# Performance work log

Measured on AMD Instinct MI355X. Metric: run time of the kernel, lower is better.

The kernel has to match this reference:

```python
import jax, jax.numpy as jnp
import numpy as np

B, L, W = 64, 20, 48
D = W * W           # 2304, MoE input/output size (image_width**2)
E = 4               # num_experts
HID = 2 * D         # expert hidden size
K = 1               # top_k
LOSS_COEF = 1e-2


def _cv_squared(x):
    # torch: x.var() (unbiased) / (x.mean()**2 + eps)
    eps = 1e-10
    return jnp.var(x, ddof=1) / (jnp.mean(x) ** 2 + eps)


def _moe(x, w_gate, w1, b1, w2, b2):
    # Noisy top-k gating, inference path (train=False => clean logits, no noise).
    logits = x @ w_gate                                   # [B, E]
    top_logits, top_idx = jax.lax.top_k(logits, K + 1)    # min(k+1, E)
    topk_gates = jax.nn.softmax(top_logits[:, :K], axis=-1)
    gates = jnp.zeros_like(logits).at[
        jnp.arange(x.shape[0])[:, None], top_idx[:, :K]
    ].set(topk_gates)                                     # [B, E] sparse gates
    importance = gates.sum(0)
    load = (gates > 0).sum(0).astype(x.dtype)             # _gates_to_load
    aux = LOSS_COEF * (_cv_squared(importance) + _cv_squared(load))
    # Dense expert compute weighted by gates (same math as dispatch/combine).
    h = jax.nn.relu(jnp.einsum('bd,edh->beh', x, w1) + b1)      # [B,E,HID]
    y = jnp.einsum('beh,ehd->bed', h, w2) + b2                  # [B,E,D]
    out = jnp.einsum('be,bed->bd', gates, y)                    # [B,D]
    return out, aux


def _conv3d(x, w, b, pad):
    y = jax.lax.conv_general_dilated(
        x, w, window_strides=(1, 1, 1), padding=pad,
        dimension_numbers=('NCDHW', 'OIDHW', 'NCDHW'))
    return y + b[None, :, None, None, None]


def _forward(input, conv1_w, conv1_b, conv2_w, conv2_b,
             t_gate, t_w1, t_b1, t_w2, t_b2,
             a_gate, a_w1, a_b1, a_w2, a_b2,
             q_gate, q_w1, q_b1, q_w2, q_b2,
             enc_w, enc_b, dec_w, dec_b):
    x = jnp.transpose(input, (0, 2, 1, 3, 4))                   # [B,1,L,H,W]
    x = jax.nn.relu(_conv3d(x, conv1_w, conv1_b, ((1, 1), (1, 1), (1, 1))))
    x = jax.nn.relu(_conv3d(x, conv2_w, conv2_b, ((0, 0), (1, 1), (1, 1))))  # [B,1,1,H,W]
    xf = x.reshape(x.shape[0], -1)                              # [B, D]
    transform, l1 = _moe(xf, t_gate, t_w1, t_b1, t_w2, t_b2)
    add, l2 = _moe(xf, a_gate, a_w1, a_b1, a_w2, a_b2)
    quad, l3 = _moe(xf, q_gate, q_w1, q_b1, q_w2, q_b2)
    s = input.shape                                             # [B,L,1,H,W]
    transform = transform.reshape(s[0], 1, s[2], s[3], s[4])
    add = add.reshape(s[0], 1, s[2], s[3], s[4])
    quad = quad.reshape(s[0], 1, s[2], s[3], s[4])
    out = input * input * quad + input * transform + add        # [B,L,1,H,W]
    # encoder = Linear(D,D)+ReLU, decoder = Linear(D,D) over flattened H*W
    of = out.reshape(s[0], s[1], D)
    of = jax.nn.relu(of @ enc_w + enc_b)
    of = of @ dec_w + dec_b
    of = jax.nn.sigmoid(of)
    return of.reshape(s), l1 + l2 + l3


def setup_inputs() -> dict:
    key = jax.random.key(0)
    ks = jax.random.split(key, 32)
    sc = 0.02
    inp = {
        'input': jax.random.normal(ks[0], (B, L, 1, W, W), jnp.float32),
        'conv1_w': jax.random.normal(ks[1], (10, 1, 3, 3, 3), jnp.float32) * sc,
        'conv1_b': jnp.zeros((10,), jnp.float32),
        'conv2_w': jax.random.normal(ks[2], (1, 10, L, 3, 3), jnp.float32) * sc,
        'conv2_b': jnp.zeros((1,), jnp.float32),
        'enc_w': jax.random.normal(ks[3], (D, D), jnp.float32) * sc,
        'enc_b': jnp.zeros((D,), jnp.float32),
        'dec_w': jax.random.normal(ks[4], (D, D), jnp.float32) * sc,
        'dec_b': jnp.zeros((D,), jnp.float32),
    }
    for i, p in enumerate(['t', 'a', 'q']):
        k0, k1, k2 = jax.random.split(ks[5 + i], 3)
        inp[p + '_gate'] = jnp.zeros((D, E), jnp.float32) + jax.random.normal(k0, (D, E), jnp.float32) * sc
        inp[p + '_w1'] = jax.random.normal(k1, (E, D, HID), jnp.float32) * sc
        inp[p + '_b1'] = jnp.zeros((E, HID), jnp.float32)
        inp[p + '_w2'] = jax.random.normal(k2, (E, HID, D), jnp.float32) * sc
        inp[p + '_b2'] = jnp.zeros((E, D), jnp.float32)
    return inp


def reference(input, conv1_w, conv1_b, conv2_w, conv2_b,
              t_gate, t_w1, t_b1, t_w2, t_b2,
              a_gate, a_w1, a_b1, a_w2, a_b2,
              q_gate, q_w1, q_b1, q_w2, q_b2,
              enc_w, enc_b, dec_w, dec_b):
    return _forward(input, conv1_w, conv1_b, conv2_w, conv2_b,
                    t_gate, t_w1, t_b1, t_w2, t_b2,
                    a_gate, a_w1, a_b1, a_w2, a_b2,
                    q_gate, q_w1, q_b1, q_w2, q_b2,
                    enc_w, enc_b, dec_w, dec_b)
```

## Files before the change

kernel.cpp:

```cpp
#include <hip/hip_runtime.h>
#include <stdint.h>

#define NB 64
#define NL 20
#define ND 2304
#define NE 4
#define NH 4608
#define NM 1280

typedef float f32x4 __attribute__((ext_vector_type(4)));
typedef __bf16 bf16x8 __attribute__((ext_vector_type(8)));
typedef unsigned short u16;
typedef u16 u16x4 __attribute__((ext_vector_type(4)));
typedef unsigned int u32;
typedef u32 u32x4 __attribute__((ext_vector_type(4)));

__device__ __forceinline__ u16 f2bf(float f) {
  u32 u = __builtin_bit_cast(u32, f);
  u += 0x7fffu + ((u >> 16) & 1u);
  return (u16)(u >> 16);
}

__device__ __forceinline__ void gl_lds16(const void* g, void* l) {
  __builtin_amdgcn_global_load_lds(
      (const __attribute__((address_space(1))) void*)g,
      (__attribute__((address_space(3))) void*)l, 16, 0, 0);
}

#define OFF_XFACC 0
#define OFF_XF    147456
#define OFF_H     294912
#define OFF_Y     1179648
#define OFF_AUX   1622016
#define OFF_CNT   1622020
#define OFF_ROWS  1622032
#define OFF_OFB   1622240
#define OFF_H1B   3096800
#define OFF_ENCWB 4571360
#define OFF_DECWB 7225568
#define OFF_XC    9879776
#define OFF_P     10322144

__global__ __launch_bounds__(256) void k_zero(float* __restrict__ p) {
  p[(size_t)blockIdx.x * 256 + threadIdx.x] = 0.f;
}

__global__ __launch_bounds__(256) void k_conv(
    const float* __restrict__ in, const float* __restrict__ w1,
    const float* __restrict__ b1, const float* __restrict__ w2,
    float* __restrict__ xf_acc) {
  __shared__ float insl[3][50][50];
  __shared__ float c1[2][50][50];
  __shared__ float w1s[270];
  __shared__ float w2s[90];
  __shared__ float b1s[10];
  const int d = blockIdx.x, b = blockIdx.y, t = threadIdx.x;
  for (int i = t; i < 270; i += 256) w1s[i] = w1[i];
  for (int i = t; i < 90; i += 256) w2s[i] = w2[(size_t)((i / 9) * 20 + d) * 9 + (i % 9)];
  if (t < 10) b1s[t] = b1[t];
  for (int i = t; i < 7500; i += 256) {
    int s = i / 2500, rr = (i % 2500) / 50, cc = i % 50;
    int gd = d - 1 + s, gy = rr - 1, gx = cc - 1;
    float v = 0.f;
    if (gd >= 0 && gd < NL && (unsigned)gy < 48u && (unsigned)gx < 48u)
      v = in[((size_t)b * NL + gd) * ND + gy * 48 + gx];
    insl[s][rr][cc] = v;
  }
  for (int i = t; i < 5000; i += 256) ((float*)c1)[i] = 0.f;
  float s2[3][4];
#pragma unroll
  for (int qi = 0; qi < 3; ++qi)
#pragma unroll
    for (int xq = 0; xq < 4; ++xq) s2[qi][xq] = 0.f;
  __syncthreads();
  for (int pc = 0; pc < 5; ++pc) {
#pragma unroll
    for (int qi = 0; qi < 3; ++qi) {
      int q = t + qi * 256;
      if (q < 576) {
        int y = q / 12, x0 = (q % 12) * 4;
        float a0[4], a1[4];
        const float bb0 = b1s[2 * pc], bb1 = b1s[2 * pc + 1];
#pragma unroll
        for (int xq = 0; xq < 4; ++xq) { a0[xq] = bb0; a1[xq] = bb1; }
#pragma unroll
        for (int kd = 0; kd < 3; ++kd)
#pragma unroll
          for (int ky = 0; ky < 3; ++ky) {
            float v[6];
#pragma unroll
            for (int i = 0; i < 6; ++i) v[i] = insl[kd][y + ky][x0 + i];
            const float* wa = &w1s[(2 * pc) * 27 + kd * 9 + ky * 3];
            const float* wb = wa + 27;
#pragma unroll
            for (int xq = 0; xq < 4; ++xq) {
              a0[xq] += v[xq] * wa[0] + v[xq + 1] * wa[1] + v[xq + 2] * wa[2];
              a1[xq] += v[xq] * wb[0] + v[xq + 1] * wb[1] + v[xq + 2] * wb[2];
            }
          }
#pragma unroll
        for (int xq = 0; xq < 4; ++xq) {
          c1[0][y + 1][x0 + 1 + xq] = fmaxf(a0[xq], 0.f);
          c1[1][y + 1][x0 + 1 + xq] = fmaxf(a1[xq], 0.f);
        }
      }
    }
    __syncthreads();
#pragma unroll
    for (int qi = 0; qi < 3; ++qi) {
      int q = t + qi * 256;
      if (q < 576) {
        int y = q / 12, x0 = (q % 12) * 4;
#pragma unroll
        for (int cc = 0; cc < 2; ++cc) {
#pragma unroll
          for (int ky = 0; ky < 3; ++ky) {
            float v[6];
#pragma unroll
            for (int i = 0; i < 6; ++i) v[i] = c1[cc][y + ky][x0 + i];
            const float* wr = &w2s[(2 * pc + cc) * 9 + ky * 3];
#pragma unroll
            for (int xq = 0; xq < 4; ++xq)
              s2[qi][xq] += v[xq] * wr[0] + v[xq + 1] * wr[1] + v[xq + 2] * wr[2];
          }
        }
      }
    }
    __syncthreads();
  }
#pragma unroll
  for (int qi = 0; qi < 3; ++qi) {
    int q = t + qi * 256;
    if (q < 576) {
#pragma unroll
      for (int xq = 0; xq < 4; ++xq)
        atomicAdd(&xf_acc[(size_t)b * ND + q * 4 + xq], s2[qi][xq]);
    }
  }
}

__global__ __launch_bounds__(256) void k_bias_relu(
    const float* __restrict__ acc, const float* __restrict__ c2b, float* __restrict__ xf) {
  size_t i = (size_t)blockIdx.x * 256 + threadIdx.x;
  xf[i] = fmaxf(acc[i] + c2b[0], 0.f);
}

__global__ __launch_bounds__(256) void k_gate(
    const float* __restrict__ xf,
    const float* __restrict__ g0, const float* __restrict__ g1, const float* __restrict__ g2,
    float* __restrict__ aux, int* __restrict__ cnt, int* __restrict__ rows) {
  const int p = blockIdx.x, t = threadIdx.x;
  const float* __restrict__ g = (p == 0) ? g0 : ((p == 1) ? g1 : g2);
  __shared__ float lg[64][4];
  __shared__ int lidx[64];
  __shared__ int lcnt[4];
  if (t < 4) lcnt[t] = 0;
  const int wv = t >> 6, l = t & 63;
  for (int b0 = 0; b0 < 64; b0 += 4) {
    int bb = b0 + wv;
    f32x4 acc = {0.f, 0.f, 0.f, 0.f};
    const float* xr = xf + (size_t)bb * ND + l * 36;
    const float* gr = g + (size_t)l * 36 * 4;
#pragma unroll
    for (int i4 = 0; i4 < 9; ++i4) {
      f32x4 xv = *(const f32x4*)(xr + i4 * 4);
#pragma unroll
      for (int qq = 0; qq < 4; ++qq) {
        f32x4 gv = *(const f32x4*)(gr + (i4 * 4 + qq) * 4);
        acc += xv[qq] * gv;
      }
    }
#pragma unroll
    for (int e = 0; e < 4; ++e) {
      float pv = acc[e];
#pragma unroll
      for (int off = 32; off > 0; off >>= 1) pv += __shfl_down(pv, off);
      if (l == 0) lg[bb][e] = pv;
    }
  }
  __syncthreads();
  if (t < 64) {
    float best = lg[t][0];
    int bi = 0;
#pragma unroll
    for (int e = 1; e < 4; ++e)
      if (lg[t][e] > best) { best = lg[t][e]; bi = e; }
    lidx[t] = bi;
    atomicAdd(&lcnt[bi], 1);
  }
  __syncthreads();
  if (t == 0) {
    int ofs[4]; int run = 0;
#pragma unroll
    for (int e = 0; e < 4; ++e) { ofs[e] = run; run += lcnt[e]; cnt[p * 4 + e] = lcnt[e]; }
    for (int b = 0; b < 64; ++b) { int e = lidx[b]; rows[p * 64 + ofs[e]++] = b; }
    float var = 0.f;
#pragma unroll
    for (int e = 0; e < 4; ++e) { float dd = (float)lcnt[e] - 16.f; var += dd * dd; }
    var *= (1.f / 3.f);
    aux[p] = 0.02f * var / (256.f + 1e-10f);
  }
}

__global__ __launch_bounds__(256) void k_gather(
    const float* __restrict__ xf, const int* __restrict__ rows, u16* __restrict__ Xb) {
  const int slot = blockIdx.x, t = threadIdx.x;
  const int r = rows[slot];
  const f32x4* src = (const f32x4*)(xf + (size_t)r * ND);
  u16x4* dst = (u16x4*)(Xb + (size_t)slot * ND);
  for (int i = t; i < ND / 4; i += 256) {
    f32x4 v = src[i];
    u16x4 o;
#pragma unroll
    for (int q = 0; q < 4; ++q) o[q] = f2bf(v[q]);
    dst[i] = o;
  }
}

template <int K, int N, int KS>
__global__ __launch_bounds__(256) void k_moe_mfma(
    const u16* __restrict__ Xb,
    const float* __restrict__ wt, const float* __restrict__ wa, const float* __restrict__ wq,
    const int* __restrict__ cnt, float* __restrict__ P) {
  constexpr int KL = K / KS;
  constexpr int NT = KL / 32;
  const int tile = blockIdx.x;
  const int ks = blockIdx.y;
  const int pe = blockIdx.z >> 1, ch = blockIdx.z & 1;
  const int p = pe >> 2, e = pe & 3;
  const int c = cnt[p * 4 + e];
  const int rstart = ch * 32;
  if (rstart >= c) return;
  const int nrows = min(32, c - rstart);
  int pref = 0;
  for (int e2 = 0; e2 < e; ++e2) pref += cnt[p * 4 + e2];
  const int slot0 = p * 64 + pref + rstart;
  const float* __restrict__ W = (p == 0) ? wt : ((p == 1) ? wa : wq);
  __shared__ u16 xs[32 * 296];
  __shared__ u16 Bs[2][128 * 40];
  const int t = threadIdx.x;
  const int w = t >> 6, l = t & 63;
  const int l15 = l & 15, l4 = l >> 4;

  if (l < 36) {
#pragma unroll
    for (int rr = 0; rr < 8; ++rr) {
      const int r = w * 8 + rr;
      int slot = slot0 + r; if (slot > 191) slot = 191;
      gl_lds16(Xb + (size_t)slot * K + ks * KL + l * 8, &xs[r * 296]);
    }
  }

  const int wk = t >> 3;
  const int wn = (t & 7) * 16;
  const float* Wg = W + (size_t)e * K * N + ((size_t)(ks * KL + wk)) * N + tile * 128 + wn;

  f32x4 rbuf[2][4];
#define LOADW(BUF, KT)                                                        \
  { _Pragma("unroll")                                                         \
    for (int q = 0; q < 4; ++q)                                               \
      rbuf[BUF][q] = *(const f32x4*)(Wg + (size_t)(KT) * 32 * N + q * 4); }
#define CVTW(BUF, DBUF)                                                       \
  { _Pragma("unroll")                                                         \
    for (int q = 0; q < 4; ++q) {                                             \
      _Pragma("unroll")                                                       \
      for (int j = 0; j < 4; ++j) {                                           \
        const int n_ = wn + q * 4 + j;                                        \
        const int pk_ = wk ^ (((n_ >> 4) & 3) << 3);                          \
        Bs[DBUF][n_ * 40 + pk_] = f2bf(rbuf[BUF][q][j]);                      \
      } } }

  f32x4 acc[4] = {};
  const int mbase = (w & 1) * 16;
  const int nql = (w >> 1) * 64;

  LOADW(0, 0);
  CVTW(0, 0);
  LOADW(1, 1);
  __syncthreads();

#pragma unroll
  for (int kt = 0; kt < NT; ++kt) {
    const bf16x8 af = *(const bf16x8*)&xs[(mbase + l15) * 296 + kt * 32 + l4 * 8];
#pragma unroll
    for (int i = 0; i < 4; ++i) {
      const int s = ((((w >> 1) * 4 + i)) & 3) << 3;
      const bf16x8 bf = *(const bf16x8*)&Bs[kt & 1][(nql + i * 16 + l15) * 40 + ((l4 * 8) ^ s)];
      acc[i] = __builtin_amdgcn_mfma_f32_16x16x32_bf16(af, bf, acc[i], 0, 0, 0);
    }
    if (kt + 1 < NT) { CVTW((kt + 1) & 1, (kt + 1) & 1); }
    if (kt + 2 < NT) { LOADW(kt & 1, kt + 2); }
    __syncthreads();
  }
#undef LOADW
#undef CVTW

  const size_t pbase = (size_t)ks * 192 * N;
#pragma unroll
  for (int i = 0; i < 4; ++i) {
    const int n = tile * 128 + nql + i * 16 + l15;
#pragma unroll
    for (int r = 0; r < 4; ++r) {
      const int m = mbase + l4 * 4 + r;
      if (m < nrows) P[pbase + (size_t)(slot0 + m) * N + n] = acc[i][r];
    }
  }
}

__global__ __launch_bounds__(256) void k_red1(
    const float* __restrict__ P,
    const float* __restrict__ b1t, const float* __restrict__ b1a, const float* __restrict__ b1q,
    const int* __restrict__ cnt, u16* __restrict__ Hb) {
  const int slot = blockIdx.y;
  const int p = slot >> 6, pos = slot & 63;
  int e = 0, run = cnt[p * 4];
  while (pos >= run && e < 3) { ++e; run += cnt[p * 4 + e]; }
  const float* __restrict__ b1 = (p == 0) ? b1t : ((p == 1) ? b1a : b1q);
  const int j0 = blockIdx.x * 1024 + threadIdx.x * 4;
  if (j0 >= NH) return;
  f32x4 s = *(const f32x4*)(b1 + (size_t)e * NH + j0);
#pragma unroll
  for (int ks = 0; ks < 8; ++ks)
    s += *(const f32x4*)(P + ((size_t)ks * 192 + slot) * NH + j0);
  u16x4 o;
#pragma unroll
  for (int q = 0; q < 4; ++q) o[q] = f2bf(fmaxf(s[q], 0.f));
  *(u16x4*)(Hb + (size_t)slot * NH + j0) = o;
}

__global__ __launch_bounds__(256) void k_red2(
    const float* __restrict__ P,
    const float* __restrict__ b2t, const float* __restrict__ b2a, const float* __restrict__ b2q,
    const int* __restrict__ cnt, const int* __restrict__ rows, float* __restrict__ Y) {
  const int slot = blockIdx.y;
  const int p = slot >> 6, pos = slot & 63;
  int e = 0, run = cnt[p * 4];
  while (pos >= run && e < 3) { ++e; run += cnt[p * 4 + e]; }
  const float* __restrict__ b2 = (p == 0) ? b2t : ((p == 1) ? b2a : b2q);
  const int b = rows[slot];
  const int t = threadIdx.x;
  if (t >= 192) return;
  const int j0 = blockIdx.x * 768 + t * 4;
  f32x4 s = *(const f32x4*)(b2 + (size_t)e * ND + j0);
#pragma unroll
  for (int ks = 0; ks < 16; ++ks)
    s += *(const f32x4*)(P + ((size_t)ks * 192 + slot) * ND + j0);
  *(f32x4*)(Y + (size_t)(p * 64 + b) * ND + j0) = s;
}

__global__ __launch_bounds__(256) void k_combine(
    const float* __restrict__ in, const float* __restrict__ Y, u16* __restrict__ ofb) {
  const size_t i = (size_t)blockIdx.x * 256 + threadIdx.x;
  const size_t e0 = i * 4;
  const int row = (int)(e0 / ND);
  const int d = (int)(e0 - (size_t)row * ND);
  const int b = row / NL;
  f32x4 v = *(const f32x4*)(in + e0);
  const size_t yb = (size_t)b * ND + d;
  f32x4 tt = *(const f32x4*)(Y + yb);
  f32x4 aa = *(const f32x4*)(Y + (size_t)64 * ND + yb);
  f32x4 qq = *(const f32x4*)(Y + (size_t)128 * ND + yb);
  u16x4 o;
#pragma unroll
  for (int q = 0; q < 4; ++q) {
    float f = v[q] * v[q] * qq[q] + v[q] * tt[q] + aa[q];
    o[q] = f2bf(f);
  }
  *(u16x4*)(ofb + e0) = o;
}

__global__ __launch_bounds__(256) void k_wt(
    const float* __restrict__ encw, const float* __restrict__ decw,
    u16* __restrict__ encb, u16* __restrict__ decb) {
  __shared__ float tl[32][33];
  const float* __restrict__ src = blockIdx.z ? decw : encw;
  u16* __restrict__ dst = blockIdx.z ? decb : encb;
  const int k0 = blockIdx.x * 32, n0 = blockIdx.y * 32;
  const int tx = threadIdx.x & 31, ty = threadIdx.x >> 5;
  for (int r = ty; r < 32; r += 8) tl[r][tx] = src[(size_t)(k0 + r) * ND + n0 + tx];
  __syncthreads();
  for (int r = ty; r < 32; r += 8) dst[(size_t)(n0 + r) * ND + k0 + tx] = f2bf(tl[tx][r]);
}

template <int MODE>
__global__ __launch_bounds__(256) void k_gemm(
    const u16* __restrict__ A, const u16* __restrict__ Bt,
    const float* __restrict__ bias, void* __restrict__ outp,
    const float* __restrict__ aux) {
  __shared__ u16 As[128 * 32];
  __shared__ u16 Bs[128 * 32];
  const int t = threadIdx.x;
  const int bm = blockIdx.x, bn = blockIdx.y;
  const int lane = t & 63;
  const int wr = (t >> 7) & 1, wc = (t >> 6) & 1;
  const int l15 = lane & 15, l4 = lane >> 4;
  f32x4 acc[4][4] = {};
  const int r0 = t >> 2, kc0 = (t & 3) * 8;
  const int r1 = (t + 256) >> 2, kc1 = ((t + 256) & 3) * 8;
  const size_t baseA = (size_t)(bm * 128) * ND;
  const size_t baseB = (size_t)(bn * 128) * ND;
  for (int k0 = 0; k0 < ND; k0 += 32) {
    *(u32x4*)(As + t * 8) = *(const u32x4*)(A + baseA + (size_t)r0 * ND + k0 + kc0);
    *(u32x4*)(Bs + t * 8) = *(const u32x4*)(Bt + baseB + (size_t)r0 * ND + k0 + kc0);
    *(u32x4*)(As + (t + 256) * 8) = *(const u32x4*)(A + baseA + (size_t)r1 * ND + k0 + kc1);
    *(u32x4*)(Bs + (t + 256) * 8) = *(const u32x4*)(Bt + baseB + (size_t)r1 * ND + k0 + kc1);
    __syncthreads();
    bf16x8 af[4], bfr[4];
#pragma unroll
    for (int i = 0; i < 4; ++i) {
      af[i] = *(const bf16x8*)(As + (wr * 64 + i * 16 + l15) * 32 + l4 * 8);
      bfr[i] = *(const bf16x8*)(Bs + (wc * 64 + i * 16 + l15) * 32 + l4 * 8);
    }
#pragma unroll
    for (int mi = 0; mi < 4; ++mi)
#pragma unroll
      for (int ni = 0; ni < 4; ++ni)
        acc[mi][ni] = __builtin_amdgcn_mfma_f32_16x16x32_bf16(af[mi], bfr[ni], acc[mi][ni], 0, 0, 0);
    __syncthreads();
  }
  const int colbase = bn * 128 + wc * 64;
  const int rowbase = bm * 128 + wr * 64;
#pragma unroll
  for (int mi = 0; mi < 4; ++mi) {
#pragma unroll
    for (int ni = 0; ni < 4; ++ni) {
      const int colg = colbase + ni * 16 + l15;
      const float bv = bias[colg];
#pragma unroll
      for (int r = 0; r < 4; ++r) {
        const int rowg = rowbase + mi * 16 + l4 * 4 + r;
        float v = acc[mi][ni][r] + bv;
        if (MODE == 0) {
          ((u16*)outp)[(size_t)rowg * ND + colg] = f2bf(fmaxf(v, 0.f));
        } else {
          ((float*)outp)[(size_t)rowg * ND + colg] = 1.f / (1.f + __expf(-v));
        }
      }
    }
  }
  if (MODE == 1 && bm == 0 && bn == 0 && t == 0)
    ((float*)outp)[(size_t)NM * ND] = aux[0] + aux[1] + aux[2];
}

extern "C" void kernel_launch(void* const* d_in, const int* in_sizes, int n_in,
                              void* d_out, int out_size, void* d_ws, size_t ws_size,
                              hipStream_t stream) {
  (void)in_sizes; (void)n_in; (void)out_size; (void)ws_size;
  const float* input   = (const float*)d_in[0];
  const float* conv1_w = (const float*)d_in[1];
  const float* conv1_b = (const float*)d_in[2];
  const float* conv2_w = (const float*)d_in[3];
  const float* conv2_b = (const float*)d_in[4];
  const float* enc_w   = (const float*)d_in[5];
  const float* enc_b   = (const float*)d_in[6];
  const float* dec_w   = (const float*)d_in[7];
  const float* dec_b   = (const float*)d_in[8];
  const float* gate_t = (const float*)d_in[9];
  const float* w1_t   = (const float*)d_in[10];
  const float* b1_t   = (const float*)d_in[11];
  const float* w2_t   = (const float*)d_in[12];
  const float* b2_t   = (const float*)d_in[13];
  const float* gate_a = (const float*)d_in[14];
  const float* w1_a   = (const float*)d_in[15];
  const float* b1_a   = (const float*)d_in[16];
  const float* w2_a   = (const float*)d_in[17];
  const float* b2_a   = (const float*)d_in[18];
  const float* gate_q = (const float*)d_in[19];
  const float* w1_q   = (const float*)d_in[20];
  const float* b1_q   = (const float*)d_in[21];
  const float* w2_q   = (const float*)d_in[22];
  const float* b2_q   = (const float*)d_in[23];

  float* ws = (float*)d_ws;
  float* xf_acc = ws + OFF_XFACC;
  float* xf     = ws + OFF_XF;
  u16*   Hb     = (u16*)(ws + OFF_H);
  float* Y      = ws + OFF_Y;
  float* aux    = ws + OFF_AUX;
  int*   cnt    = (int*)(ws + OFF_CNT);
  int*   rows   = (int*)(ws + OFF_ROWS);
  u16*   ofb    = (u16*)(ws + OFF_OFB);
  u16*   h1b    = (u16*)(ws + OFF_H1B);
  u16*   encwb  = (u16*)(ws + OFF_ENCWB);
  u16*   decwb  = (u16*)(ws + OFF_DECWB);
  u16*   Xcb    = (u16*)(ws + OFF_XC);
  float* P      = ws + OFF_P;

  k_zero<<<576, 256, 0, stream>>>(xf_acc);
  k_conv<<<dim3(20, 64), 256, 0, stream>>>(input, conv1_w, conv1_b, conv2_w, xf_acc);
  k_bias_relu<<<576, 256, 0, stream>>>(xf_acc, conv2_b, xf);
  k_wt<<<dim3(72, 72, 2), 256, 0, stream>>>(enc_w, dec_w, encwb, decwb);
  k_gate<<<3, 256, 0, stream>>>(xf, gate_t, gate_a, gate_q, aux, cnt, rows);
  k_gather<<<192, 256, 0, stream>>>(xf, rows, Xcb);
  k_moe_mfma<ND, NH, 8><<<dim3(36, 8, 24), 256, 0, stream>>>(Xcb, w1_t, w1_a, w1_q, cnt, P);
  k_red1<<<dim3(5, 192), 256, 0, stream>>>(P, b1_t, b1_a, b1_q, cnt, Hb);
  k_moe_mfma<NH, ND, 16><<<dim3(18, 16, 24), 256, 0, stream>>>(Hb, w2_t, w2_a, w2_q, cnt, P);
  k_red2<<<dim3(3, 192), 256, 0, stream>>>(P, b2_t, b2_a, b2_q, cnt, rows, Y);
  k_combine<<<2880, 256, 0, stream>>>(input, Y, ofb);
  k_gemm<0><<<dim3(10, 18), 256, 0, stream>>>(ofb, encwb, enc_b, (void*)h1b, aux);
  k_gemm<1><<<dim3(10, 18), 256, 0, stream>>>(h1b, decwb, dec_b, d_out, aux);
}
```

Before: 559.4 us.

## Stream fp32 expert weights directly to LDS with 4-stage pipeline, shrink tiles

The MoE expert GEMM now copies fp32 weight tiles straight into shared memory with global_load_lds across four buffers, three tiles in flight. Each thread converts to bf16 when building its MFMA operand, replacing the register-load, convert and scattered LDS-store path. The N tile shrinks from 128 to 64, and the dense enc/dec GEMMs move from 128-row to 64-row M tiles, doubling block counts to raise occupancy on the many CUs. The costs are more LDS traffic, strided scalar LDS reads for the B fragment, and less reuse per block.

```diff
diff --git a/kernel.cpp b/kernel.cpp
--- a/kernel.cpp
+++ b/kernel.cpp
@@ -237,7 +237,7 @@
   const int slot0 = p * 64 + pref + rstart;
   const float* __restrict__ W = (p == 0) ? wt : ((p == 1) ? wa : wq);
   __shared__ u16 xs[32 * 296];
-  __shared__ u16 Bs[2][128 * 40];
+  __shared__ float wb[4][32 * 64];
   const int t = threadIdx.x;
   const int w = t >> 6, l = t & 63;
   const int l15 = l & 15, l4 = l >> 4;
@@ -250,55 +250,46 @@
       gl_lds16(Xb + (size_t)slot * K + ks * KL + l * 8, &xs[r * 296]);
     }
   }
-
-  const int wk = t >> 3;
-  const int wn = (t & 7) * 16;
-  const float* Wg = W + (size_t)e * K * N + ((size_t)(ks * KL + wk)) * N + tile * 128 + wn;
-
-  f32x4 rbuf[2][4];
-#define LOADW(BUF, KT)                                                        \
+  const float* Wg = W + (size_t)e * K * N + (size_t)(ks * KL) * N + tile * 64;
+#define STAGEW(BUF, KT)                                                       \
   { _Pragma("unroll")                                                         \
-    for (int q = 0; q < 4; ++q)                                               \
-      rbuf[BUF][q] = *(const f32x4*)(Wg + (size_t)(KT) * 32 * N + q * 4); }
-#define CVTW(BUF, DBUF)                                                       \
-  { _Pragma("unroll")                                                         \
-    for (int q = 0; q < 4; ++q) {                                             \
-      _Pragma("unroll")                                                       \
-      for (int j = 0; j < 4; ++j) {                                           \
-        const int n_ = wn + q * 4 + j;                                        \
-        const int pk_ = wk ^ (((n_ >> 4) & 3) << 3);                          \
-        Bs[DBUF][n_ * 40 + pk_] = f2bf(rbuf[BUF][q][j]);                      \
-      } } }
-
-  f32x4 acc[4] = {};
+    for (int j = 0; j < 2; ++j)                                               \
+      gl_lds16(Wg + ((size_t)((KT) * 32 + w * 8 + j * 4 + l4)) * N + l15 * 4, \
+               &wb[BUF][(w * 8 + j * 4) * 64]); }
+
+  f32x4 acc[2] = {};
   const int mbase = (w & 1) * 16;
-  const int nql = (w >> 1) * 64;
-
-  LOADW(0, 0);
-  CVTW(0, 0);
-  LOADW(1, 1);
+  const int nb0 = (w >> 1) * 32;
+
+  STAGEW(0, 0); STAGEW(1, 1); STAGEW(2, 2);
+  asm volatile("s_waitcnt vmcnt(0)" ::: "memory");
   __syncthreads();
 
 #pragma unroll
   for (int kt = 0; kt < NT; ++kt) {
+    if (kt + 3 < NT) STAGEW((kt + 3) & 3, kt + 3);
     const bf16x8 af = *(const bf16x8*)&xs[(mbase + l15) * 296 + kt * 32 + l4 * 8];
-#pragma unroll
-    for (int i = 0; i < 4; ++i) {
-      const int s = ((((w >> 1) * 4 + i)) & 3) << 3;
-      const bf16x8 bf = *(const bf16x8*)&Bs[kt & 1][(nql + i * 16 + l15) * 40 + ((l4 * 8) ^ s)];
-      acc[i] = __builtin_amdgcn_mfma_f32_16x16x32_bf16(af, bf, acc[i], 0, 0, 0);
-    }
-    if (kt + 1 < NT) { CVTW((kt + 1) & 1, (kt + 1) & 1); }
-    if (kt + 2 < NT) { LOADW(kt & 1, kt + 2); }
+    const float* ww = &wb[kt & 3][0];
+#pragma unroll
+    for (int i = 0; i < 2; ++i) {
+      const int nb = nb0 + i * 16 + l15;
+      bf16x8 bfr;
+#pragma unroll
+      for (int j = 0; j < 8; ++j)
+        bfr[j] = (__bf16)ww[(l4 * 8 + j) * 64 + nb];
+      acc[i] = __builtin_amdgcn_mfma_f32_16x16x32_bf16(af, bfr, acc[i], 0, 0, 0);
+    }
+    if (kt + 3 < NT)      { asm volatile("s_waitcnt vmcnt(4)" ::: "memory"); }
+    else if (kt + 2 < NT) { asm volatile("s_waitcnt vmcnt(2)" ::: "memory"); }
+    else if (kt + 1 < NT) { asm volatile("s_waitcnt vmcnt(0)" ::: "memory"); }
     __syncthreads();
   }
-#undef LOADW
-#undef CVTW
+#undef STAGEW
 
   const size_t pbase = (size_t)ks * 192 * N;
 #pragma unroll
-  for (int i = 0; i < 4; ++i) {
-    const int n = tile * 128 + nql + i * 16 + l15;
+  for (int i = 0; i < 2; ++i) {
+    const int n = tile * 64 + nb0 + i * 16 + l15;
 #pragma unroll
     for (int r = 0; r < 4; ++r) {
       const int m = mbase + l4 * 4 + r;
@@ -387,41 +378,41 @@
     const u16* __restrict__ A, const u16* __restrict__ Bt,
     const float* __restrict__ bias, void* __restrict__ outp,
     const float* __restrict__ aux) {
-  __shared__ u16 As[128 * 32];
+  __shared__ u16 As[64 * 32];
   __shared__ u16 Bs[128 * 32];
   const int t = threadIdx.x;
   const int bm = blockIdx.x, bn = blockIdx.y;
   const int lane = t & 63;
   const int wr = (t >> 7) & 1, wc = (t >> 6) & 1;
   const int l15 = lane & 15, l4 = lane >> 4;
-  f32x4 acc[4][4] = {};
+  f32x4 acc[2][4] = {};
   const int r0 = t >> 2, kc0 = (t & 3) * 8;
   const int r1 = (t + 256) >> 2, kc1 = ((t + 256) & 3) * 8;
-  const size_t baseA = (size_t)(bm * 128) * ND;
+  const size_t baseA = (size_t)(bm * 64) * ND;
   const size_t baseB = (size_t)(bn * 128) * ND;
   for (int k0 = 0; k0 < ND; k0 += 32) {
     *(u32x4*)(As + t * 8) = *(const u32x4*)(A + baseA + (size_t)r0 * ND + k0 + kc0);
     *(u32x4*)(Bs + t * 8) = *(const u32x4*)(Bt + baseB + (size_t)r0 * ND + k0 + kc0);
-    *(u32x4*)(As + (t + 256) * 8) = *(const u32x4*)(A + baseA + (size_t)r1 * ND + k0 + kc1);
     *(u32x4*)(Bs + (t + 256) * 8) = *(const u32x4*)(Bt + baseB + (size_t)r1 * ND + k0 + kc1);
     __syncthreads();
-    bf16x8 af[4], bfr[4];
-#pragma unroll
-    for (int i = 0; i < 4; ++i) {
-      af[i] = *(const bf16x8*)(As + (wr * 64 + i * 16 + l15) * 32 + l4 * 8);
+    bf16x8 af[2], bfr[4];
+#pragma unroll
+    for (int i = 0; i < 2; ++i)
+      af[i] = *(const bf16x8*)(As + (wr * 32 + i * 16 + l15) * 32 + l4 * 8);
+#pragma unroll
+    for (int i = 0; i < 4; ++i)
       bfr[i] = *(const bf16x8*)(Bs + (wc * 64 + i * 16 + l15) * 32 + l4 * 8);
-    }
-#pragma unroll
-    for (int mi = 0; mi < 4; ++mi)
+#pragma unroll
+    for (int mi = 0; mi < 2; ++mi)
 #pragma unroll
       for (int ni = 0; ni < 4; ++ni)
         acc[mi][ni] = __builtin_amdgcn_mfma_f32_16x16x32_bf16(af[mi], bfr[ni], acc[mi][ni], 0, 0, 0);
     __syncthreads();
   }
   const int colbase = bn * 128 + wc * 64;
-  const int rowbase = bm * 128 + wr * 64;
-#pragma unroll
-  for (int mi = 0; mi < 4; ++mi) {
+  const int rowbase = bm * 64 + wr * 32;
+#pragma unroll
+  for (int mi = 0; mi < 2; ++mi) {
 #pragma unroll
     for (int ni = 0; ni < 4; ++ni) {
       const int colg = colbase + ni * 16 + l15;
@@ -492,11 +483,11 @@
   k_wt<<<dim3(72, 72, 2), 256, 0, stream>>>(enc_w, dec_w, encwb, decwb);
   k_gate<<<3, 256, 0, stream>>>(xf, gate_t, gate_a, gate_q, aux, cnt, rows);
   k_gather<<<192, 256, 0, stream>>>(xf, rows, Xcb);
-  k_moe_mfma<ND, NH, 8><<<dim3(36, 8, 24), 256, 0, stream>>>(Xcb, w1_t, w1_a, w1_q, cnt, P);
+  k_moe_mfma<ND, NH, 8><<<dim3(72, 8, 24), 256, 0, stream>>>(Xcb, w1_t, w1_a, w1_q, cnt, P);
   k_red1<<<dim3(5, 192), 256, 0, stream>>>(P, b1_t, b1_a, b1_q, cnt, Hb);
-  k_moe_mfma<NH, ND, 16><<<dim3(18, 16, 24), 256, 0, stream>>>(Hb, w2_t, w2_a, w2_q, cnt, P);
+  k_moe_mfma<NH, ND, 16><<<dim3(36, 16, 24), 256, 0, stream>>>(Hb, w2_t, w2_a, w2_q, cnt, P);
   k_red2<<<dim3(3, 192), 256, 0, stream>>>(P, b2_t, b2_a, b2_q, cnt, rows, Y);
   k_combine<<<2880, 256, 0, stream>>>(input, Y, ofb);
-  k_gemm<0><<<dim3(10, 18), 256, 0, stream>>>(ofb, encwb, enc_b, (void*)h1b, aux);
-  k_gemm<1><<<dim3(10, 18), 256, 0, stream>>>(h1b, decwb, dec_b, d_out, aux);
-}
+  k_gemm<0><<<dim3(20, 18), 256, 0, stream>>>(ofb, encwb, enc_b, (void*)h1b, aux);
+  k_gemm<1><<<dim3(20, 18), 256, 0, stream>>>(h1b, decwb, dec_b, d_out, aux);
+}
```

Result: faster. 530.9 us (-5.1%).
